# Kernel tuning notes

Hardware: AMD Instinct MI355X
Metric: run time of the kernel (lower is better)

Reference implementation:

```python
import jax, jax.numpy as jnp
import numpy as np

B, N, C_IN = 8, 2048, 3
D = 64            # graph-conv feature dim
SPARSE_K = 8      # k_neighbors(16) * sparse_ratio(0.5)
LEVELS = 3        # wavelet_levels
H1, H2 = 256, 128 # fusion hidden dims

def _lin(key, fan_in, fan_out):
    k1, k2 = jax.random.split(key)
    s = 1.0 / np.sqrt(fan_in)
    W = jax.random.uniform(k1, (fan_in, fan_out), minval=-s, maxval=s, dtype=jnp.float32)
    b = jax.random.uniform(k2, (fan_out,), minval=-s, maxval=s, dtype=jnp.float32)
    return W, b

def setup_inputs() -> dict:
    key = jax.random.key(0)
    ks = jax.random.split(key, 12)
    x = jax.random.normal(ks[0], (B, N, C_IN), dtype=jnp.float32)
    W1, b1 = _lin(ks[1], C_IN, D)          # feature_transform
    W2, b2 = _lin(ks[2], 2 * D, D)         # edge_conv
    Ws1, bs1 = _lin(ks[3], C_IN, 64)       # suppressor layer 1
    Ws2, bs2 = _lin(ks[4], 64, LEVELS)     # suppressor layer 2
    Wf1, bf1 = _lin(ks[5], D * LEVELS, H1) # fusion
    Wf2, bf2 = _lin(ks[6], H1, H2)
    Wf3, bf3 = _lin(ks[7], H2, C_IN)
    ones = jnp.ones; zeros = jnp.zeros
    return {
        'x': x,
        'W1': W1, 'b1': b1, 'g1': ones((D,), jnp.float32), 'be1': zeros((D,), jnp.float32),
        'W2': W2, 'b2': b2, 'g2': ones((D,), jnp.float32), 'be2': zeros((D,), jnp.float32),
        'Ws1': Ws1, 'bs1': bs1, 'Ws2': Ws2, 'bs2': bs2,
        'Wf1': Wf1, 'bf1': bf1, 'gf1': ones((H1,), jnp.float32), 'bef1': zeros((H1,), jnp.float32),
        'Wf2': Wf2, 'bf2': bf2, 'gf2': ones((H2,), jnp.float32), 'bef2': zeros((H2,), jnp.float32),
        'Wf3': Wf3, 'bf3': bf3,
    }

def _leaky(v):
    return jnp.where(v > 0, v, 0.2 * v)

def reference(x, W1, b1, g1, be1, W2, b2, g2, be2, Ws1, bs1, Ws2, bs2,
              Wf1, bf1, gf1, bef1, Wf2, bf2, gf2, bef2, Wf3, bf3):
    # ---- AdaptiveSparseGraphConv ----
    # feature transform + eval-mode BN (running mean 0 / var 1 -> affine)
    feat = _leaky((x @ W1 + b1) * g1 + be1)                     # [B,N,D]
    # KNN via squared distances (monotonic in true cdist)
    x2 = jnp.sum(x * x, axis=-1)                                # [B,N]
    d2 = x2[:, :, None] + x2[:, None, :] - 2.0 * jnp.einsum('bnc,bmc->bnm', x, x)
    _, idx = jax.lax.top_k(-d2, SPARSE_K)                       # [B,N,k] nearest
    neighbor = jax.vmap(lambda f, i: f[i])(feat, idx)           # [B,N,k,D]
    edge = jnp.concatenate(
        [jnp.broadcast_to(feat[:, :, None, :], neighbor.shape), neighbor], axis=-1)  # [B,N,k,2D]
    conv = _leaky((edge @ W2 + b2) * g2 + be2)                  # [B,N,k,D]
    agg = jnp.max(conv, axis=2)                                 # [B,N,D]
    # ---- AdaptiveFrequencySupressor (per-point wavelet-level weights) ----
    fw = jax.nn.sigmoid(jax.nn.relu(x @ Ws1 + bs1) @ Ws2 + bs2) # [B,N,LEVELS]
    # frequency-adaptive multi-level weighting, concat across levels
    multi = (agg[:, :, None, :] * fw[:, :, :, None]).reshape(B, N, LEVELS * D)  # [B,N,LEVELS*D]
    # ---- EnhancedMultiScaleFusion (eval: dropout off, BN affine) ----
    h = _leaky((multi @ Wf1 + bf1) * gf1 + bef1)
    h = _leaky((h @ Wf2 + bf2) * gf2 + bef2)
    delta = h @ Wf3 + bf3                                       # [B,N,3]
    # ---- residual regularized output ----
    return x + 0.1 * delta
```

## Files before the change

### kernel.cpp

```cpp
#include <hip/hip_runtime.h>
#include <math.h>

#define BB   8
#define NN   2048
#define BN   16384
#define KNB  8

__device__ __forceinline__ float leaky(float v){ return v > 0.f ? v : 0.2f*v; }

__device__ __forceinline__ ushort f2bf(float f){
    unsigned u = __float_as_uint(f);
    return (ushort)((u + 0x7FFFu + ((u >> 16) & 1u)) >> 16);
}
__device__ __forceinline__ float bf2f(ushort h){
    return __uint_as_float(((unsigned)h) << 16);
}

using bf16x8 = __attribute__((ext_vector_type(8))) short;
using f32x4  = __attribute__((ext_vector_type(4)))  float;

#define CEF(a, b) { float mn_ = fminf(a,b), mx_ = fmaxf(a,b); (a) = mn_; (b) = mx_; }

__global__ __launch_bounds__(1024, 8) void k_front(
    const float* __restrict__ x,
    const float* __restrict__ W1, const float* __restrict__ b1,
    const float* __restrict__ g1, const float* __restrict__ be1,
    const float* __restrict__ W2,
    const float* __restrict__ Wf1, const float* __restrict__ Wf2,
    float* __restrict__ P, ushort* __restrict__ Qb,
    ushort* __restrict__ Wf1T, ushort* __restrict__ Wf2T,
    int* __restrict__ idxo)
{
    __shared__ __align__(16) char smem[51584];
    int t = threadIdx.x;
    int bid = blockIdx.x;

    if (bid < 256) {
        float* F_s = (float*)smem;
        float* W_s = (float*)(smem + 16896);
        int rb = bid * 64;

        {
            int d = t & 63, g = t >> 6;
            float w0 = W1[d], w1 = W1[64+d], w2 = W1[128+d];
            float bb = b1[d], gg = g1[d], ee = be1[d];
            #pragma unroll
            for (int i = 0; i < 4; ++i) {
                int r = g*4 + i;
                const float* xp = &x[(rb + r)*3];
                float f = xp[0]*w0 + xp[1]*w1 + xp[2]*w2 + bb;
                F_s[r*66 + d] = leaky(f*gg + ee);
            }
        }

        int tx = t & 15, ty = t >> 4;
        float acc[8];
        #pragma unroll
        for (int j = 0; j < 8; ++j) acc[j] = 0.f;

        for (int k0 = 0; k0 < 64; k0 += 32) {
            __syncthreads();
            {
                int k = t >> 5, c4 = (t & 31) * 4;
                const float* src = &W2[(k0 + k + (c4 >= 64 ? 64 : 0))*64 + (c4 & 63)];
                *(float4*)&W_s[k*132 + c4] = *(const float4*)src;
            }
            __syncthreads();
            #pragma unroll 8
            for (int kk = 0; kk < 32; ++kk) {
                float a = F_s[ty*66 + k0 + kk];
                float4 wA = *(const float4*)&W_s[kk*132 + tx*8];
                float4 wB = *(const float4*)&W_s[kk*132 + tx*8 + 4];
                acc[0] = fmaf(a, wA.x, acc[0]);
                acc[1] = fmaf(a, wA.y, acc[1]);
                acc[2] = fmaf(a, wA.z, acc[2]);
                acc[3] = fmaf(a, wA.w, acc[3]);
                acc[4] = fmaf(a, wB.x, acc[4]);
                acc[5] = fmaf(a, wB.y, acc[5]);
                acc[6] = fmaf(a, wB.z, acc[6]);
                acc[7] = fmaf(a, wB.w, acc[7]);
            }
        }

        int r = rb + ty;
        if (tx < 8) {
            *(float4*)&P[r*64 + tx*8]     = make_float4(acc[0], acc[1], acc[2], acc[3]);
            *(float4*)&P[r*64 + tx*8 + 4] = make_float4(acc[4], acc[5], acc[6], acc[7]);
        } else {
            union { ushort u[8]; uint4 v; } pk;
            #pragma unroll
            for (int j = 0; j < 8; ++j) pk.u[j] = f2bf(acc[j]);
            *(uint4*)&Qb[r*64 + (tx - 8)*8] = pk.v;
        }
        return;
    }

    if (bid < 266) {
        if (bid < 262) {
            int base = (bid - 256) * 8192 + t * 8;
            #pragma unroll
            for (int j = 0; j < 8; ++j) {
                int e = base + j;
                int n = e / 192, k = e % 192;
                Wf1T[e] = f2bf(Wf1[k*256 + n]);
            }
        } else {
            int base = (bid - 262) * 8192 + t * 8;
            #pragma unroll
            for (int j = 0; j < 8; ++j) {
                int e = base + j;
                int n = e >> 8, k = e & 255;
                Wf2T[e] = f2bf(Wf2[k*128 + n]);
            }
        }
        return;
    }

    float4* sp    = (float4*)smem;
    float*  mg    = (float*) (smem + 32768);
    float*  v8buf = (float*) (smem + 49152);
    int*    eqbuf = (int*)   (smem + 49280);
    int*    cnt   = (int*)   (smem + 51328);
    int*    ecnt  = (int*)   (smem + 51456);

    int kbid = bid - 266;
    int b = kbid >> 6;
    int qbase = (kbid & 63) * 32;
    int q = t & 31, seg = t >> 5;
    int w = t >> 6, lane = t & 63;

    for (int i = t; i < NN; i += 1024) {
        float a = x[(b*NN + i)*3 + 0];
        float c = x[(b*NN + i)*3 + 1];
        float e = x[(b*NN + i)*3 + 2];
        sp[i] = make_float4(a, c, e, a*a + c*c + e*e);
    }
    __syncthreads();

    float4 qv = sp[qbase + q];
    float R[8];
    #pragma unroll
    for (int j = 0; j < 8; ++j) R[j] = 1e30f;

    int m0 = seg * 64;
    #pragma unroll 2
    for (int g = 0; g < 8; ++g) {
        float S[8];
        #pragma unroll
        for (int jj = 0; jj < 8; ++jj) {
            int m = m0 + g*8 + jj;
            float4 v = sp[m];
            float s = qv.x*v.x; s = fmaf(qv.y, v.y, s); s = fmaf(qv.z, v.z, s);
            float d2 = fmaf(-2.f, s, qv.w + v.w);
            S[jj] = fmaxf(d2, 0.f);
        }
        CEF(S[0],S[1]); CEF(S[2],S[3]); CEF(S[4],S[5]); CEF(S[6],S[7]);
        CEF(S[0],S[2]); CEF(S[1],S[3]); CEF(S[4],S[6]); CEF(S[5],S[7]);
        CEF(S[1],S[2]); CEF(S[5],S[6]);
        CEF(S[0],S[4]); CEF(S[1],S[5]); CEF(S[2],S[6]); CEF(S[3],S[7]);
        CEF(S[2],S[4]); CEF(S[3],S[5]);
        CEF(S[1],S[2]); CEF(S[3],S[4]); CEF(S[5],S[6]);
        #pragma unroll
        for (int j = 0; j < 8; ++j) R[j] = fminf(R[j], S[7-j]);
        CEF(R[0],R[4]); CEF(R[1],R[5]); CEF(R[2],R[6]); CEF(R[3],R[7]);
        CEF(R[0],R[2]); CEF(R[1],R[3]); CEF(R[4],R[6]); CEF(R[5],R[7]);
        CEF(R[0],R[1]); CEF(R[2],R[3]); CEF(R[4],R[5]); CEF(R[6],R[7]);
    }

    {
        float Rp[8];
        #pragma unroll
        for (int j = 0; j < 8; ++j) Rp[j] = __shfl_xor(R[j], 32, 64);
        float C[8];
        #pragma unroll
        for (int j = 0; j < 8; ++j) C[j] = fminf(R[j], Rp[7-j]);
        CEF(C[0],C[4]); CEF(C[1],C[5]); CEF(C[2],C[6]); CEF(C[3],C[7]);
        CEF(C[0],C[2]); CEF(C[1],C[3]); CEF(C[4],C[6]); CEF(C[5],C[7]);
        CEF(C[0],C[1]); CEF(C[2],C[3]); CEF(C[4],C[5]); CEF(C[6],C[7]);
        if (lane < 32) {
            #pragma unroll
            for (int j = 0; j < 8; ++j) mg[(w*32 + lane)*8 + j] = C[j];
        }
    }

    #pragma unroll
    for (int lvl = 0; lvl < 4; ++lvl) {
        int Pn = 8 >> lvl;
        int sh = 3 - lvl;
        bool active = (t < 32*Pn);
        float C[8];
        int qq = 0, p = 0;
        __syncthreads();
        if (active) {
            qq = t >> sh; p = t & (Pn - 1);
            float A[8], Bv[8];
            #pragma unroll
            for (int j = 0; j < 8; ++j) {
                A[j]  = mg[((2*p)*32 + qq)*8 + j];
                Bv[j] = mg[((2*p + 1)*32 + qq)*8 + j];
            }
            #pragma unroll
            for (int j = 0; j < 8; ++j) C[j] = fminf(A[j], Bv[7-j]);
            CEF(C[0],C[4]); CEF(C[1],C[5]); CEF(C[2],C[6]); CEF(C[3],C[7]);
            CEF(C[0],C[2]); CEF(C[1],C[3]); CEF(C[4],C[6]); CEF(C[5],C[7]);
            CEF(C[0],C[1]); CEF(C[2],C[3]); CEF(C[4],C[5]); CEF(C[6],C[7]);
        }
        __syncthreads();
        if (active) {
            if (Pn > 1) {
                #pragma unroll
                for (int j = 0; j < 8; ++j) mg[(p*32 + qq)*8 + j] = C[j];
            } else {
                v8buf[qq] = C[7];
            }
        }
    }
    if (t >= 32 && t < 64)  cnt[t - 32] = 0;
    if (t >= 64 && t < 96)  ecnt[t - 64] = 0;
    __syncthreads();

    {
        float v8 = v8buf[q];
        int obase = (b*NN + qbase + q)*KNB;
        #pragma unroll 4
        for (int jj = 0; jj < 64; ++jj) {
            int m = m0 + jj;
            float4 v = sp[m];
            float s = qv.x*v.x; s = fmaf(qv.y, v.y, s); s = fmaf(qv.z, v.z, s);
            float d2 = fmaf(-2.f, s, qv.w + v.w);
            d2 = fmaxf(d2, 0.f);
            if (d2 <= v8) {
                if (d2 < v8) {
                    int slot = atomicAdd(&cnt[q], 1);
                    idxo[obase + slot] = b*NN + m;
                } else {
                    int slot = atomicAdd(&ecnt[q], 1);
                    if (slot < 16) eqbuf[q*16 + slot] = m;
                }
            }
        }
    }
    __syncthreads();

    if (t < 32) {
        int qq = t;
        int cLT = cnt[qq];
        int ne = ecnt[qq]; if (ne > 16) ne = 16;
        int need = 8 - cLT;
        int obase = (b*NN + qbase + qq)*KNB;
        for (int k = 0; k < need; ++k) {
            int best = 0x7FFFFFFF, bi = -1;
            for (int i = 0; i < ne; ++i) {
                int v = eqbuf[qq*16 + i];
                if (v < best) { best = v; bi = i; }
            }
            if (bi >= 0) {
                eqbuf[qq*16 + bi] = 0x7FFFFFFF;
                idxo[obase + cLT + k] = b*NN + best;
            }
        }
    }
}

__global__ __launch_bounds__(256, 4) void k_fuse(
    const float* __restrict__ x,
    const float* __restrict__ P, const ushort* __restrict__ Qb,
    const int* __restrict__ idx,
    const float* __restrict__ Ws1, const float* __restrict__ bs1,
    const float* __restrict__ Ws2, const float* __restrict__ bs2,
    const float* __restrict__ b2, const float* __restrict__ g2,
    const float* __restrict__ be2,
    const ushort* __restrict__ Wf1T, const float* __restrict__ bf1,
    const float* __restrict__ gf1, const float* __restrict__ bef1,
    const ushort* __restrict__ Wf2T, const float* __restrict__ bf2,
    const float* __restrict__ gf2, const float* __restrict__ bef2,
    const float* __restrict__ Wf3, const float* __restrict__ bf3,
    float* __restrict__ out)
{
    __shared__ __align__(16) char smem[9216];
    ushort* A_s  = (ushort*)smem;
    ushort* h1_s = (ushort*)smem;
    float*  pd   = (float*) (smem + 8448);

    int t = threadIdx.x, w = t >> 6, lane = t & 63;
    int rb = blockIdx.x * 16;
    int l15 = lane & 15, kg = lane >> 4, kb = kg * 8;

    {
        float ws1a = Ws1[lane], ws1b = Ws1[64+lane], ws1c = Ws1[128+lane];
        float bs1v = bs1[lane];
        float ws2a = Ws2[lane*3+0], ws2b = Ws2[lane*3+1], ws2c = Ws2[lane*3+2];
        float bs20 = bs2[0], bs21 = bs2[1], bs22 = bs2[2];
        float g2v = g2[lane], be2v = be2[lane], b2v = b2[lane];

        int p0 = rb + w*4;
        float Pv[4]; int nb[4][8];
        #pragma unroll
        for (int i = 0; i < 4; ++i) {
            Pv[i] = P[(p0 + i)*64 + lane] + b2v;
            #pragma unroll
            for (int j = 0; j < 8; ++j) nb[i][j] = idx[(p0 + i)*8 + j];
        }
        #pragma unroll
        for (int i = 0; i < 4; ++i) {
            int p = p0 + i;
            float qg[8];
            #pragma unroll
            for (int j = 0; j < 8; ++j) qg[j] = bf2f(Qb[nb[i][j]*64 + lane]);
            float x0 = x[p*3+0], x1 = x[p*3+1], x2 = x[p*3+2];
            float h = fmaxf(fmaf(x2, ws1c, fmaf(x1, ws1b, fmaf(x0, ws1a, bs1v))), 0.f);
            float s0 = h*ws2a, s1 = h*ws2b, s2 = h*ws2c;
            #pragma unroll
            for (int off = 32; off; off >>= 1) {
                s0 += __shfl_xor(s0, off, 64);
                s1 += __shfl_xor(s1, off, 64);
                s2 += __shfl_xor(s2, off, 64);
            }
            float fw0 = 1.f/(1.f + expf(-(s0 + bs20)));
            float fw1 = 1.f/(1.f + expf(-(s1 + bs21)));
            float fw2 = 1.f/(1.f + expf(-(s2 + bs22)));
            float mx = -1e30f;
            #pragma unroll
            for (int j = 0; j < 8; ++j)
                mx = fmaxf(mx, leaky((Pv[i] + qg[j])*g2v + be2v));
            int r = w*4 + i;
            A_s[r*200 + lane]       = f2bf(mx * fw0);
            A_s[r*200 + 64 + lane]  = f2bf(mx * fw1);
            A_s[r*200 + 128 + lane] = f2bf(mx * fw2);
        }
    }
    __syncthreads();

    f32x4 acc[4];
    #pragma unroll
    for (int n2 = 0; n2 < 4; ++n2)
        #pragma unroll
        for (int i = 0; i < 4; ++i) acc[n2][i] = 0.f;

    {
        const ushort* Bb = Wf1T + (w*64 + l15)*192 + kb;
        #pragma unroll
        for (int k0 = 0; k0 < 192; k0 += 32) {
            bf16x8 a = *(const bf16x8*)&A_s[l15*200 + k0 + kb];
            #pragma unroll
            for (int n2 = 0; n2 < 4; ++n2) {
                bf16x8 b = *(const bf16x8*)&Bb[n2*(16*192) + k0];
                acc[n2] = __builtin_amdgcn_mfma_f32_16x16x32_bf16(a, b, acc[n2], 0, 0, 0);
            }
        }
    }
    __syncthreads();

    #pragma unroll
    for (int n2 = 0; n2 < 4; ++n2) {
        int c = w*64 + n2*16 + l15;
        float bv = bf1[c], gv = gf1[c], ev = bef1[c];
        #pragma unroll
        for (int rg = 0; rg < 4; ++rg) {
            int r = kg*4 + rg;
            float v = leaky((acc[n2][rg] + bv)*gv + ev);
            h1_s[r*264 + c] = f2bf(v);
        }
    }
    __syncthreads();

    f32x4 acc2[2];
    #pragma unroll
    for (int n2 = 0; n2 < 2; ++n2)
        #pragma unroll
        for (int i = 0; i < 4; ++i) acc2[n2][i] = 0.f;

    {
        const ushort* Bb2 = Wf2T + (w*32 + l15)*256 + kb;
        #pragma unroll
        for (int k0 = 0; k0 < 256; k0 += 32) {
            bf16x8 a = *(const bf16x8*)&h1_s[l15*264 + k0 + kb];
            #pragma unroll
            for (int n2 = 0; n2 < 2; ++n2) {
                bf16x8 b = *(const bf16x8*)&Bb2[n2*(16*256) + k0];
                acc2[n2] = __builtin_amdgcn_mfma_f32_16x16x32_bf16(a, b, acc2[n2], 0, 0, 0);
            }
        }
    }

    {
        float bv[2], gv[2], ev[2], w3[2][3];
        #pragma unroll
        for (int n2 = 0; n2 < 2; ++n2) {
            int c = w*32 + n2*16 + l15;
            bv[n2] = bf2[c]; gv[n2] = gf2[c]; ev[n2] = bef2[c];
            #pragma unroll
            for (int l = 0; l < 3; ++l) w3[n2][l] = Wf3[c*3 + l];
        }
        #pragma unroll
        for (int rg = 0; rg < 4; ++rg) {
            float d0 = 0.f, d1 = 0.f, d2 = 0.f;
            #pragma unroll
            for (int n2 = 0; n2 < 2; ++n2) {
                float v = leaky((acc2[n2][rg] + bv[n2])*gv[n2] + ev[n2]);
                d0 = fmaf(v, w3[n2][0], d0);
                d1 = fmaf(v, w3[n2][1], d1);
                d2 = fmaf(v, w3[n2][2], d2);
            }
            #pragma unroll
            for (int off = 8; off; off >>= 1) {
                d0 += __shfl_xor(d0, off, 64);
                d1 += __shfl_xor(d1, off, 64);
                d2 += __shfl_xor(d2, off, 64);
            }
            int r = kg*4 + rg;
            if (l15 < 3) {
                float dl = (l15 == 0) ? d0 : (l15 == 1 ? d1 : d2);
                pd[(r*4 + w)*3 + l15] = dl;
            }
        }
    }
    __syncthreads();

    if (t < 48) {
        int r = t / 3, l = t - r*3;
        float delta = pd[(r*4 + 0)*3 + l] + pd[(r*4 + 1)*3 + l]
                    + pd[(r*4 + 2)*3 + l] + pd[(r*4 + 3)*3 + l] + bf3[l];
        out[(rb + r)*3 + l] = x[(rb + r)*3 + l] + 0.1f*delta;
    }
}

extern "C" void kernel_launch(void* const* d_in, const int* in_sizes, int n_in,
                              void* d_out, int out_size, void* d_ws, size_t ws_size,
                              hipStream_t stream)
{
    const float* x    = (const float*)d_in[0];
    const float* W1   = (const float*)d_in[1];
    const float* b1   = (const float*)d_in[2];
    const float* g1   = (const float*)d_in[3];
    const float* be1  = (const float*)d_in[4];
    const float* W2   = (const float*)d_in[5];
    const float* b2   = (const float*)d_in[6];
    const float* g2   = (const float*)d_in[7];
    const float* be2  = (const float*)d_in[8];
    const float* Ws1  = (const float*)d_in[9];
    const float* bs1  = (const float*)d_in[10];
    const float* Ws2  = (const float*)d_in[11];
    const float* bs2  = (const float*)d_in[12];
    const float* Wf1  = (const float*)d_in[13];
    const float* bf1  = (const float*)d_in[14];
    const float* gf1  = (const float*)d_in[15];
    const float* bef1 = (const float*)d_in[16];
    const float* Wf2  = (const float*)d_in[17];
    const float* bf2  = (const float*)d_in[18];
    const float* gf2  = (const float*)d_in[19];
    const float* bef2 = (const float*)d_in[20];
    const float* Wf3  = (const float*)d_in[21];
    const float* bf3  = (const float*)d_in[22];
    float* out = (float*)d_out;

    char* ws = (char*)d_ws;
    int*    idx   = (int*)   (ws + 0);
    ushort* Wf1T  = (ushort*)(ws + (1u << 20));
    ushort* Wf2T  = (ushort*)(ws + (1u << 20) + (512u << 10));
    float*  P     = (float*) (ws + (2u  << 20));
    ushort* Qb    = (ushort*)(ws + (6u  << 20));

    k_front<<<778, 1024, 0, stream>>>(x, W1, b1, g1, be1, W2, Wf1, Wf2,
                                      P, Qb, Wf1T, Wf2T, idx);
    k_fuse<<<BN/16, 256, 0, stream>>>(x, P, Qb, idx, Ws1, bs1, Ws2, bs2, b2, g2, be2,
                                      Wf1T, bf1, gf1, bef1, Wf2T, bf2, gf2, bef2,
                                      Wf3, bf3, out);
}
```

Measured before the change: 157.7 us.

## Pack distance and index into 64-bit keys for single-pass KNN top-k

The KNN selection now sorts 64-bit keys that hold the float distance bits in the high word and the point index in the low word. This lets the merge tree emit the indices directly and removes the second distance-recompute pass, the shared-memory atomics and the serial tie-break loop. The cost is that every compare-exchange and shuffle now works on 64-bit values, which roughly doubles the register and ALU work of the sorting network. The merge buffer grows to a packed 13-word stride per entry.

```diff
diff --git a/kernel.cpp b/kernel.cpp
--- a/kernel.cpp
+++ b/kernel.cpp
@@ -1,5 +1,6 @@
 #include <hip/hip_runtime.h>
 #include <math.h>
+#include <stdint.h>
 
 #define BB   8
 #define NN   2048
@@ -19,7 +20,8 @@
 using bf16x8 = __attribute__((ext_vector_type(8))) short;
 using f32x4  = __attribute__((ext_vector_type(4)))  float;
 
-#define CEF(a, b) { float mn_ = fminf(a,b), mx_ = fmaxf(a,b); (a) = mn_; (b) = mx_; }
+#define CEK(a, b) { bool c_ = (a) < (b); uint64_t mn_ = c_?(a):(b), mx_ = c_?(b):(a); (a) = mn_; (b) = mx_; }
+#define MINK(a, b) { if ((b) < (a)) (a) = (b); }
 
 __global__ __launch_bounds__(1024, 8) void k_front(
     const float* __restrict__ x,
@@ -31,7 +33,7 @@
     ushort* __restrict__ Wf1T, ushort* __restrict__ Wf2T,
     int* __restrict__ idxo)
 {
-    __shared__ __align__(16) char smem[51584];
+    __shared__ __align__(16) char smem[59392];
     int t = threadIdx.x;
     int bid = blockIdx.x;
 
@@ -116,12 +118,8 @@
         return;
     }
 
-    float4* sp    = (float4*)smem;
-    float*  mg    = (float*) (smem + 32768);
-    float*  v8buf = (float*) (smem + 49152);
-    int*    eqbuf = (int*)   (smem + 49280);
-    int*    cnt   = (int*)   (smem + 51328);
-    int*    ecnt  = (int*)   (smem + 51456);
+    float4* sp  = (float4*)smem;
+    uint*   mgv = (uint*)  (smem + 32768);
 
     int kbid = bid - 266;
     int b = kbid >> 6;
@@ -138,125 +136,94 @@
     __syncthreads();
 
     float4 qv = sp[qbase + q];
-    float R[8];
+    uint64_t R[8];
     #pragma unroll
-    for (int j = 0; j < 8; ++j) R[j] = 1e30f;
+    for (int j = 0; j < 8; ++j) R[j] = ~0ull;
 
     int m0 = seg * 64;
     #pragma unroll 2
     for (int g = 0; g < 8; ++g) {
-        float S[8];
+        uint64_t S[8];
         #pragma unroll
         for (int jj = 0; jj < 8; ++jj) {
             int m = m0 + g*8 + jj;
             float4 v = sp[m];
             float s = qv.x*v.x; s = fmaf(qv.y, v.y, s); s = fmaf(qv.z, v.z, s);
             float d2 = fmaf(-2.f, s, qv.w + v.w);
-            S[jj] = fmaxf(d2, 0.f);
-        }
-        CEF(S[0],S[1]); CEF(S[2],S[3]); CEF(S[4],S[5]); CEF(S[6],S[7]);
-        CEF(S[0],S[2]); CEF(S[1],S[3]); CEF(S[4],S[6]); CEF(S[5],S[7]);
-        CEF(S[1],S[2]); CEF(S[5],S[6]);
-        CEF(S[0],S[4]); CEF(S[1],S[5]); CEF(S[2],S[6]); CEF(S[3],S[7]);
-        CEF(S[2],S[4]); CEF(S[3],S[5]);
-        CEF(S[1],S[2]); CEF(S[3],S[4]); CEF(S[5],S[6]);
-        #pragma unroll
-        for (int j = 0; j < 8; ++j) R[j] = fminf(R[j], S[7-j]);
-        CEF(R[0],R[4]); CEF(R[1],R[5]); CEF(R[2],R[6]); CEF(R[3],R[7]);
-        CEF(R[0],R[2]); CEF(R[1],R[3]); CEF(R[4],R[6]); CEF(R[5],R[7]);
-        CEF(R[0],R[1]); CEF(R[2],R[3]); CEF(R[4],R[5]); CEF(R[6],R[7]);
+            d2 = fmaxf(d2, 0.f);
+            S[jj] = ((uint64_t)__float_as_uint(d2) << 32) | (uint32_t)m;
+        }
+        CEK(S[0],S[1]); CEK(S[2],S[3]); CEK(S[4],S[5]); CEK(S[6],S[7]);
+        CEK(S[0],S[2]); CEK(S[1],S[3]); CEK(S[4],S[6]); CEK(S[5],S[7]);
+        CEK(S[1],S[2]); CEK(S[5],S[6]);
+        CEK(S[0],S[4]); CEK(S[1],S[5]); CEK(S[2],S[6]); CEK(S[3],S[7]);
+        CEK(S[2],S[4]); CEK(S[3],S[5]);
+        CEK(S[1],S[2]); CEK(S[3],S[4]); CEK(S[5],S[6]);
+        #pragma unroll
+        for (int j = 0; j < 8; ++j) { MINK(R[j], S[7-j]); }
+        CEK(R[0],R[4]); CEK(R[1],R[5]); CEK(R[2],R[6]); CEK(R[3],R[7]);
+        CEK(R[0],R[2]); CEK(R[1],R[3]); CEK(R[4],R[6]); CEK(R[5],R[7]);
+        CEK(R[0],R[1]); CEK(R[2],R[3]); CEK(R[4],R[5]); CEK(R[6],R[7]);
     }
 
     {
-        float Rp[8];
-        #pragma unroll
-        for (int j = 0; j < 8; ++j) Rp[j] = __shfl_xor(R[j], 32, 64);
-        float C[8];
-        #pragma unroll
-        for (int j = 0; j < 8; ++j) C[j] = fminf(R[j], Rp[7-j]);
-        CEF(C[0],C[4]); CEF(C[1],C[5]); CEF(C[2],C[6]); CEF(C[3],C[7]);
-        CEF(C[0],C[2]); CEF(C[1],C[3]); CEF(C[4],C[6]); CEF(C[5],C[7]);
-        CEF(C[0],C[1]); CEF(C[2],C[3]); CEF(C[4],C[5]); CEF(C[6],C[7]);
+        uint64_t C[8];
+        #pragma unroll
+        for (int j = 0; j < 8; ++j) {
+            uint64_t Rp = __shfl_xor((unsigned long long)R[7-j], 32, 64);
+            C[j] = R[j] < Rp ? R[j] : Rp;
+        }
+        CEK(C[0],C[4]); CEK(C[1],C[5]); CEK(C[2],C[6]); CEK(C[3],C[7]);
+        CEK(C[0],C[2]); CEK(C[1],C[3]); CEK(C[4],C[6]); CEK(C[5],C[7]);
+        CEK(C[0],C[1]); CEK(C[2],C[3]); CEK(C[4],C[5]); CEK(C[6],C[7]);
         if (lane < 32) {
-            #pragma unroll
-            for (int j = 0; j < 8; ++j) mg[(w*32 + lane)*8 + j] = C[j];
+            int e = w*32 + lane;
+            #pragma unroll
+            for (int j = 0; j < 8; ++j) {
+                mgv[e*13 + j] = (uint)(C[j] >> 32);
+                ((ushort*)&mgv[e*13 + 8])[j] = (ushort)C[j];
+            }
         }
     }
 
     #pragma unroll
     for (int lvl = 0; lvl < 4; ++lvl) {
         int Pn = 8 >> lvl;
-        int sh = 3 - lvl;
         bool active = (t < 32*Pn);
-        float C[8];
+        uint64_t C[8];
         int qq = 0, p = 0;
         __syncthreads();
         if (active) {
-            qq = t >> sh; p = t & (Pn - 1);
-            float A[8], Bv[8];
+            qq = t & 31; p = t >> 5;
+            int e1 = (2*p)*32 + qq, e2 = (2*p + 1)*32 + qq;
+            uint64_t A[8];
             #pragma unroll
             for (int j = 0; j < 8; ++j) {
-                A[j]  = mg[((2*p)*32 + qq)*8 + j];
-                Bv[j] = mg[((2*p + 1)*32 + qq)*8 + j];
-            }
-            #pragma unroll
-            for (int j = 0; j < 8; ++j) C[j] = fminf(A[j], Bv[7-j]);
-            CEF(C[0],C[4]); CEF(C[1],C[5]); CEF(C[2],C[6]); CEF(C[3],C[7]);
-            CEF(C[0],C[2]); CEF(C[1],C[3]); CEF(C[4],C[6]); CEF(C[5],C[7]);
-            CEF(C[0],C[1]); CEF(C[2],C[3]); CEF(C[4],C[5]); CEF(C[6],C[7]);
+                A[j] = ((uint64_t)mgv[e1*13 + j] << 32) | ((ushort*)&mgv[e1*13 + 8])[j];
+            }
+            #pragma unroll
+            for (int j = 0; j < 8; ++j) {
+                uint64_t Bv = ((uint64_t)mgv[e2*13 + (7-j)] << 32) | ((ushort*)&mgv[e2*13 + 8])[7-j];
+                C[j] = A[j] < Bv ? A[j] : Bv;
+            }
+            CEK(C[0],C[4]); CEK(C[1],C[5]); CEK(C[2],C[6]); CEK(C[3],C[7]);
+            CEK(C[0],C[2]); CEK(C[1],C[3]); CEK(C[4],C[6]); CEK(C[5],C[7]);
+            CEK(C[0],C[1]); CEK(C[2],C[3]); CEK(C[4],C[5]); CEK(C[6],C[7]);
         }
         __syncthreads();
         if (active) {
             if (Pn > 1) {
+                int e = p*32 + qq;
                 #pragma unroll
-                for (int j = 0; j < 8; ++j) mg[(p*32 + qq)*8 + j] = C[j];
+                for (int j = 0; j < 8; ++j) {
+                    mgv[e*13 + j] = (uint)(C[j] >> 32);
+                    ((ushort*)&mgv[e*13 + 8])[j] = (ushort)C[j];
+                }
             } else {
-                v8buf[qq] = C[7];
-            }
-        }
-    }
-    if (t >= 32 && t < 64)  cnt[t - 32] = 0;
-    if (t >= 64 && t < 96)  ecnt[t - 64] = 0;
-    __syncthreads();
-
-    {
-        float v8 = v8buf[q];
-        int obase = (b*NN + qbase + q)*KNB;
-        #pragma unroll 4
-        for (int jj = 0; jj < 64; ++jj) {
-            int m = m0 + jj;
-            float4 v = sp[m];
-            float s = qv.x*v.x; s = fmaf(qv.y, v.y, s); s = fmaf(qv.z, v.z, s);
-            float d2 = fmaf(-2.f, s, qv.w + v.w);
-            d2 = fmaxf(d2, 0.f);
-            if (d2 <= v8) {
-                if (d2 < v8) {
-                    int slot = atomicAdd(&cnt[q], 1);
-                    idxo[obase + slot] = b*NN + m;
-                } else {
-                    int slot = atomicAdd(&ecnt[q], 1);
-                    if (slot < 16) eqbuf[q*16 + slot] = m;
-                }
-            }
-        }
-    }
-    __syncthreads();
-
-    if (t < 32) {
-        int qq = t;
-        int cLT = cnt[qq];
-        int ne = ecnt[qq]; if (ne > 16) ne = 16;
-        int need = 8 - cLT;
-        int obase = (b*NN + qbase + qq)*KNB;
-        for (int k = 0; k < need; ++k) {
-            int best = 0x7FFFFFFF, bi = -1;
-            for (int i = 0; i < ne; ++i) {
-                int v = eqbuf[qq*16 + i];
-                if (v < best) { best = v; bi = i; }
-            }
-            if (bi >= 0) {
-                eqbuf[qq*16 + bi] = 0x7FFFFFFF;
-                idxo[obase + cLT + k] = b*NN + best;
+                int obase = (b*NN + qbase + qq)*KNB;
+                #pragma unroll
+                for (int j = 0; j < 8; ++j)
+                    idxo[obase + j] = b*NN + (int)(C[j] & 0xFFFFu);
             }
         }
     }
```

New measurement: 167.1 us. 1.06x slower.

## Restructure KNN blocks to 64 queries with wave-uniform candidates read from global

Applied to the files above, without the earlier changes.

The KNN part of k_front now handles 64 queries per block instead of 32, halving the KNN block count from 512 to 256. Each wave scans a contiguous 128-candidate slice that is the same address for every lane, reading x straight from global/cache instead of staging all points into shared memory. The cross-wave shuffle merge is dropped in favour of a padded (stride 9) shared tree merge over 16 partial lists. This cuts the shared-memory staging pass and its barrier, and reduces LDS use and bank conflicts. In exchange it recomputes candidate norms and relies on scalar or broadcast global loads, with longer per-thread loops.

```diff
diff --git a/kernel.cpp b/kernel.cpp
--- a/kernel.cpp
+++ b/kernel.cpp
@@ -1,5 +1,6 @@
 #include <hip/hip_runtime.h>
 #include <math.h>
+#include <stdint.h>
 
 #define BB   8
 #define NN   2048
@@ -20,6 +21,13 @@
 using f32x4  = __attribute__((ext_vector_type(4)))  float;
 
 #define CEF(a, b) { float mn_ = fminf(a,b), mx_ = fmaxf(a,b); (a) = mn_; (b) = mx_; }
+
+__device__ __forceinline__ float dist2(float4 qv, float vx, float vy, float vz){
+    float vw = fmaf(vz, vz, fmaf(vy, vy, vx*vx));
+    float s  = qv.x*vx; s = fmaf(qv.y, vy, s); s = fmaf(qv.z, vz, s);
+    float d2 = fmaf(-2.f, s, qv.w + vw);
+    return fmaxf(d2, 0.f);
+}
 
 __global__ __launch_bounds__(1024, 8) void k_front(
     const float* __restrict__ x,
@@ -31,7 +39,7 @@
     ushort* __restrict__ Wf1T, ushort* __restrict__ Wf2T,
     int* __restrict__ idxo)
 {
-    __shared__ __align__(16) char smem[51584];
+    __shared__ __align__(16) char smem[41728];
     int t = threadIdx.x;
     int bid = blockIdx.x;
 
@@ -116,44 +124,36 @@
         return;
     }
 
-    float4* sp    = (float4*)smem;
-    float*  mg    = (float*) (smem + 32768);
-    float*  v8buf = (float*) (smem + 49152);
-    int*    eqbuf = (int*)   (smem + 49280);
-    int*    cnt   = (int*)   (smem + 51328);
-    int*    ecnt  = (int*)   (smem + 51456);
+    float* mg    = (float*)smem;
+    float* v8buf = (float*)(smem + 36864);
+    int*   eqbuf = (int*)  (smem + 37120);
+    int*   cnt   = (int*)  (smem + 41216);
+    int*   ecnt  = (int*)  (smem + 41472);
 
     int kbid = bid - 266;
-    int b = kbid >> 6;
-    int qbase = (kbid & 63) * 32;
-    int q = t & 31, seg = t >> 5;
+    int b = kbid >> 5;
+    int qbase = (kbid & 31) * 64;
     int w = t >> 6, lane = t & 63;
 
-    for (int i = t; i < NN; i += 1024) {
-        float a = x[(b*NN + i)*3 + 0];
-        float c = x[(b*NN + i)*3 + 1];
-        float e = x[(b*NN + i)*3 + 2];
-        sp[i] = make_float4(a, c, e, a*a + c*c + e*e);
-    }
-    __syncthreads();
-
-    float4 qv = sp[qbase + q];
+    float4 qv;
+    {
+        int p = b*NN + qbase + lane;
+        qv.x = x[p*3+0]; qv.y = x[p*3+1]; qv.z = x[p*3+2];
+        qv.w = fmaf(qv.z, qv.z, fmaf(qv.y, qv.y, qv.x*qv.x));
+    }
+
+    const float* cpw = &x[(b*NN + w*128)*3];
+
     float R[8];
     #pragma unroll
     for (int j = 0; j < 8; ++j) R[j] = 1e30f;
 
-    int m0 = seg * 64;
-    #pragma unroll 2
-    for (int g = 0; g < 8; ++g) {
+    for (int g = 0; g < 16; ++g) {
+        const float* cg = cpw + g*24;
         float S[8];
         #pragma unroll
-        for (int jj = 0; jj < 8; ++jj) {
-            int m = m0 + g*8 + jj;
-            float4 v = sp[m];
-            float s = qv.x*v.x; s = fmaf(qv.y, v.y, s); s = fmaf(qv.z, v.z, s);
-            float d2 = fmaf(-2.f, s, qv.w + v.w);
-            S[jj] = fmaxf(d2, 0.f);
-        }
+        for (int j = 0; j < 8; ++j)
+            S[j] = dist2(qv, cg[j*3+0], cg[j*3+1], cg[j*3+2]);
         CEF(S[0],S[1]); CEF(S[2],S[3]); CEF(S[4],S[5]); CEF(S[6],S[7]);
         CEF(S[0],S[2]); CEF(S[1],S[3]); CEF(S[4],S[6]); CEF(S[5],S[7]);
         CEF(S[1],S[2]); CEF(S[5],S[6]);
@@ -168,39 +168,26 @@
     }
 
     {
-        float Rp[8];
-        #pragma unroll
-        for (int j = 0; j < 8; ++j) Rp[j] = __shfl_xor(R[j], 32, 64);
-        float C[8];
-        #pragma unroll
-        for (int j = 0; j < 8; ++j) C[j] = fminf(R[j], Rp[7-j]);
-        CEF(C[0],C[4]); CEF(C[1],C[5]); CEF(C[2],C[6]); CEF(C[3],C[7]);
-        CEF(C[0],C[2]); CEF(C[1],C[3]); CEF(C[4],C[6]); CEF(C[5],C[7]);
-        CEF(C[0],C[1]); CEF(C[2],C[3]); CEF(C[4],C[5]); CEF(C[6],C[7]);
-        if (lane < 32) {
-            #pragma unroll
-            for (int j = 0; j < 8; ++j) mg[(w*32 + lane)*8 + j] = C[j];
-        }
-    }
+        int e = w*64 + lane;
+        #pragma unroll
+        for (int j = 0; j < 8; ++j) mg[e*9 + j] = R[j];
+    }
+    if (t >= 64 && t < 128)       cnt[t - 64]  = 0;
+    else if (t >= 128 && t < 192) ecnt[t - 128] = 0;
 
     #pragma unroll
     for (int lvl = 0; lvl < 4; ++lvl) {
         int Pn = 8 >> lvl;
-        int sh = 3 - lvl;
-        bool active = (t < 32*Pn);
+        bool active = (t < 64*Pn);
         float C[8];
         int qq = 0, p = 0;
         __syncthreads();
         if (active) {
-            qq = t >> sh; p = t & (Pn - 1);
-            float A[8], Bv[8];
-            #pragma unroll
-            for (int j = 0; j < 8; ++j) {
-                A[j]  = mg[((2*p)*32 + qq)*8 + j];
-                Bv[j] = mg[((2*p + 1)*32 + qq)*8 + j];
-            }
-            #pragma unroll
-            for (int j = 0; j < 8; ++j) C[j] = fminf(A[j], Bv[7-j]);
+            qq = t & 63; p = t >> 6;
+            int e1 = (2*p)*64 + qq, e2 = (2*p + 1)*64 + qq;
+            #pragma unroll
+            for (int j = 0; j < 8; ++j)
+                C[j] = fminf(mg[e1*9 + j], mg[e2*9 + (7-j)]);
             CEF(C[0],C[4]); CEF(C[1],C[5]); CEF(C[2],C[6]); CEF(C[3],C[7]);
             CEF(C[0],C[2]); CEF(C[1],C[3]); CEF(C[4],C[6]); CEF(C[5],C[7]);
             CEF(C[0],C[1]); CEF(C[2],C[3]); CEF(C[4],C[5]); CEF(C[6],C[7]);
@@ -208,41 +195,40 @@
         __syncthreads();
         if (active) {
             if (Pn > 1) {
+                int e = p*64 + qq;
                 #pragma unroll
-                for (int j = 0; j < 8; ++j) mg[(p*32 + qq)*8 + j] = C[j];
+                for (int j = 0; j < 8; ++j) mg[e*9 + j] = C[j];
             } else {
                 v8buf[qq] = C[7];
             }
         }
     }
-    if (t >= 32 && t < 64)  cnt[t - 32] = 0;
-    if (t >= 64 && t < 96)  ecnt[t - 64] = 0;
-    __syncthreads();
-
-    {
-        float v8 = v8buf[q];
-        int obase = (b*NN + qbase + q)*KNB;
-        #pragma unroll 4
-        for (int jj = 0; jj < 64; ++jj) {
-            int m = m0 + jj;
-            float4 v = sp[m];
-            float s = qv.x*v.x; s = fmaf(qv.y, v.y, s); s = fmaf(qv.z, v.z, s);
-            float d2 = fmaf(-2.f, s, qv.w + v.w);
-            d2 = fmaxf(d2, 0.f);
-            if (d2 <= v8) {
-                if (d2 < v8) {
-                    int slot = atomicAdd(&cnt[q], 1);
-                    idxo[obase + slot] = b*NN + m;
-                } else {
-                    int slot = atomicAdd(&ecnt[q], 1);
-                    if (slot < 16) eqbuf[q*16 + slot] = m;
+    __syncthreads();
+
+    {
+        float v8 = v8buf[lane];
+        int obase = (b*NN + qbase + lane)*KNB;
+        for (int g = 0; g < 16; ++g) {
+            const float* cg = cpw + g*24;
+            #pragma unroll
+            for (int j = 0; j < 8; ++j) {
+                float d2 = dist2(qv, cg[j*3+0], cg[j*3+1], cg[j*3+2]);
+                if (d2 <= v8) {
+                    int m = w*128 + g*8 + j;
+                    if (d2 < v8) {
+                        int slot = atomicAdd(&cnt[lane], 1);
+                        idxo[obase + slot] = b*NN + m;
+                    } else {
+                        int slot = atomicAdd(&ecnt[lane], 1);
+                        if (slot < 16) eqbuf[lane*16 + slot] = m;
+                    }
                 }
             }
         }
     }
     __syncthreads();
 
-    if (t < 32) {
+    if (t < 64) {
         int qq = t;
         int cLT = cnt[qq];
         int ne = ecnt[qq]; if (ne > 16) ne = 16;
@@ -461,7 +447,7 @@
     float*  P     = (float*) (ws + (2u  << 20));
     ushort* Qb    = (ushort*)(ws + (6u  << 20));
 
-    k_front<<<778, 1024, 0, stream>>>(x, W1, b1, g1, be1, W2, Wf1, Wf2,
+    k_front<<<522, 1024, 0, stream>>>(x, W1, b1, g1, be1, W2, Wf1, Wf2,
                                       P, Qb, Wf1T, Wf2T, idx);
     k_fuse<<<BN/16, 256, 0, stream>>>(x, P, Qb, idx, Ws1, bs1, Ws2, bs2, b2, g2, be2,
                                       Wf1T, bf1, gf1, bef1, Wf2T, bf2, gf2, bef2,
```

Result: slower. 173.1 us (+9.7%).

## Merge front-kernel role blocks so every block does GEMM, transpose, and KNN

Applied to the files above, without the earlier changes.

The front kernel previously used separate block roles: 256 blocks for the feature/W2 projection, 10 for weight transposes, and 512 for KNN. Now each of the 512 blocks handles a 32-row slice of the projection, a 160-element share of the Wf1/Wf2 bf16 transposes, and then its KNN query tile, all in one pass. The aim is to cut the launched block count and balance work so no short blocks sit beside long KNN blocks. In exchange, every block pays the projection and its barriers before starting KNN, and shared memory is reused across the phases.

```diff
diff --git a/kernel.cpp b/kernel.cpp
--- a/kernel.cpp
+++ b/kernel.cpp
@@ -1,5 +1,6 @@
 #include <hip/hip_runtime.h>
 #include <math.h>
+#include <stdint.h>
 
 #define BB   8
 #define NN   2048
@@ -35,86 +36,69 @@
     int t = threadIdx.x;
     int bid = blockIdx.x;
 
-    if (bid < 256) {
+    if (t < 160) {
+        int e = bid * 160 + t;
+        if (e < 49152) {
+            int n = e / 192, k = e % 192;
+            Wf1T[e] = f2bf(Wf1[k*256 + n]);
+        } else {
+            int e2 = e - 49152;
+            int n = e2 >> 8, k = e2 & 255;
+            Wf2T[e2] = f2bf(Wf2[k*128 + n]);
+        }
+    }
+
+    {
         float* F_s = (float*)smem;
-        float* W_s = (float*)(smem + 16896);
-        int rb = bid * 64;
+        float* W_s = (float*)(smem + 8448);
+        int rb = bid * 32;
 
         {
             int d = t & 63, g = t >> 6;
             float w0 = W1[d], w1 = W1[64+d], w2 = W1[128+d];
             float bb = b1[d], gg = g1[d], ee = be1[d];
             #pragma unroll
-            for (int i = 0; i < 4; ++i) {
-                int r = g*4 + i;
+            for (int i = 0; i < 2; ++i) {
+                int r = g*2 + i;
                 const float* xp = &x[(rb + r)*3];
                 float f = xp[0]*w0 + xp[1]*w1 + xp[2]*w2 + bb;
                 F_s[r*66 + d] = leaky(f*gg + ee);
             }
         }
-
-        int tx = t & 15, ty = t >> 4;
-        float acc[8];
-        #pragma unroll
-        for (int j = 0; j < 8; ++j) acc[j] = 0.f;
-
-        for (int k0 = 0; k0 < 64; k0 += 32) {
-            __syncthreads();
-            {
-                int k = t >> 5, c4 = (t & 31) * 4;
-                const float* src = &W2[(k0 + k + (c4 >= 64 ? 64 : 0))*64 + (c4 & 63)];
+        {
+            #pragma unroll
+            for (int it = 0; it < 2; ++it) {
+                int i2 = t + it*1024;
+                int k = i2 >> 5, c4 = (i2 & 31) * 4;
+                const float* src = &W2[(k + (c4 >= 64 ? 64 : 0))*64 + (c4 & 63)];
                 *(float4*)&W_s[k*132 + c4] = *(const float4*)src;
             }
-            __syncthreads();
-            #pragma unroll 8
-            for (int kk = 0; kk < 32; ++kk) {
-                float a = F_s[ty*66 + k0 + kk];
-                float4 wA = *(const float4*)&W_s[kk*132 + tx*8];
-                float4 wB = *(const float4*)&W_s[kk*132 + tx*8 + 4];
-                acc[0] = fmaf(a, wA.x, acc[0]);
-                acc[1] = fmaf(a, wA.y, acc[1]);
-                acc[2] = fmaf(a, wA.z, acc[2]);
-                acc[3] = fmaf(a, wA.w, acc[3]);
-                acc[4] = fmaf(a, wB.x, acc[4]);
-                acc[5] = fmaf(a, wB.y, acc[5]);
-                acc[6] = fmaf(a, wB.z, acc[6]);
-                acc[7] = fmaf(a, wB.w, acc[7]);
-            }
-        }
-
-        int r = rb + ty;
-        if (tx < 8) {
-            *(float4*)&P[r*64 + tx*8]     = make_float4(acc[0], acc[1], acc[2], acc[3]);
-            *(float4*)&P[r*64 + tx*8 + 4] = make_float4(acc[4], acc[5], acc[6], acc[7]);
+        }
+        __syncthreads();
+
+        int row = t >> 5, cg = t & 31;
+        float4 acc = make_float4(0.f, 0.f, 0.f, 0.f);
+        #pragma unroll 8
+        for (int kk = 0; kk < 64; ++kk) {
+            float a = F_s[row*66 + kk];
+            float4 wv = *(const float4*)&W_s[kk*132 + cg*4];
+            acc.x = fmaf(a, wv.x, acc.x);
+            acc.y = fmaf(a, wv.y, acc.y);
+            acc.z = fmaf(a, wv.z, acc.z);
+            acc.w = fmaf(a, wv.w, acc.w);
+        }
+
+        int r = rb + row;
+        if (cg < 16) {
+            *(float4*)&P[r*64 + cg*4] = acc;
         } else {
-            union { ushort u[8]; uint4 v; } pk;
-            #pragma unroll
-            for (int j = 0; j < 8; ++j) pk.u[j] = f2bf(acc[j]);
-            *(uint4*)&Qb[r*64 + (tx - 8)*8] = pk.v;
-        }
-        return;
-    }
-
-    if (bid < 266) {
-        if (bid < 262) {
-            int base = (bid - 256) * 8192 + t * 8;
-            #pragma unroll
-            for (int j = 0; j < 8; ++j) {
-                int e = base + j;
-                int n = e / 192, k = e % 192;
-                Wf1T[e] = f2bf(Wf1[k*256 + n]);
-            }
-        } else {
-            int base = (bid - 262) * 8192 + t * 8;
-            #pragma unroll
-            for (int j = 0; j < 8; ++j) {
-                int e = base + j;
-                int n = e >> 8, k = e & 255;
-                Wf2T[e] = f2bf(Wf2[k*128 + n]);
-            }
-        }
-        return;
-    }
+            union { ushort u[4]; uint2 v; } pk;
+            pk.u[0] = f2bf(acc.x); pk.u[1] = f2bf(acc.y);
+            pk.u[2] = f2bf(acc.z); pk.u[3] = f2bf(acc.w);
+            *(uint2*)&Qb[r*64 + (cg - 16)*4] = pk.v;
+        }
+    }
+    __syncthreads();
 
     float4* sp    = (float4*)smem;
     float*  mg    = (float*) (smem + 32768);
@@ -123,9 +107,8 @@
     int*    cnt   = (int*)   (smem + 51328);
     int*    ecnt  = (int*)   (smem + 51456);
 
-    int kbid = bid - 266;
-    int b = kbid >> 6;
-    int qbase = (kbid & 63) * 32;
+    int b = bid >> 6;
+    int qbase = (bid & 63) * 32;
     int q = t & 31, seg = t >> 5;
     int w = t >> 6, lane = t & 63;
 
@@ -461,7 +444,7 @@
     float*  P     = (float*) (ws + (2u  << 20));
     ushort* Qb    = (ushort*)(ws + (6u  << 20));
 
-    k_front<<<778, 1024, 0, stream>>>(x, W1, b1, g1, be1, W2, Wf1, Wf2,
+    k_front<<<512, 1024, 0, stream>>>(x, W1, b1, g1, be1, W2, Wf1, Wf2,
                                       P, Qb, Wf1T, Wf2T, idx);
     k_fuse<<<BN/16, 256, 0, stream>>>(x, P, Qb, idx, Ws1, bs1, Ws2, bs2, b2, g2, be2,
                                       Wf1T, bf1, gf1, bef1, Wf2T, bf2, gf2, bef2,
```

Result: no change. 155.4 us, median of 2 (-1.4%).
